# Kernel tuning notes

Measured on AMD Instinct MI355X. Metric: run time of the kernel, lower is better.

Reference implementation:

```python
import jax, jax.numpy as jnp
import numpy as np

B, S, D = 2, 2048, 2048
HQ, HKV = 32, 8
HD = D // HQ            # head_dim = 64
G = HQ // HKV           # groups = 4
KV_DIM = HKV * HD       # 512


def setup_inputs() -> dict:
    key = jax.random.key(0)
    ks = jax.random.split(key, 5)
    x = jax.random.normal(ks[0], (B, S, D), dtype=jnp.float32)
    W_q = jax.random.normal(ks[1], (D, D), dtype=jnp.float32) * (1.0 / np.sqrt(D))
    W_k = jax.random.normal(ks[2], (D, KV_DIM), dtype=jnp.float32) * (1.0 / np.sqrt(D))
    W_v = jax.random.normal(ks[3], (D, KV_DIM), dtype=jnp.float32) * (1.0 / np.sqrt(D))
    W_o = jax.random.normal(ks[4], (D, D), dtype=jnp.float32) * (1.0 / np.sqrt(D))
    # causal mask: 1 where attending allowed, 0 elsewhere (masked_fill(mask==0, -inf))
    mask = jnp.tril(jnp.ones((S, S), dtype=jnp.int32))[None, None, :, :]
    return {"x": x, "W_q": W_q, "W_k": W_k, "W_v": W_v, "W_o": W_o, "mask": mask}


def reference(x, W_q, W_k, W_v, W_o, mask):
    scale = np.sqrt(HD).astype(np.float32)
    # projections
    Q = (x @ W_q).reshape(B, S, HQ, HD).transpose(0, 2, 1, 3)    # (B,Hq,S,hd)
    K = (x @ W_k).reshape(B, S, HKV, HD).transpose(0, 2, 1, 3)   # (B,Hkv,S,hd)
    V = (x @ W_v).reshape(B, S, HKV, HD).transpose(0, 2, 1, 3)   # (B,Hkv,S,hd)
    # group Q heads with their shared KV head instead of repeat_interleave
    Qg = Q.reshape(B, HKV, G, S, HD)                             # (B,Hkv,G,S,hd)
    scores = jnp.einsum('bkgsd,bktd->bkgst', Qg, K) / scale      # (B,Hkv,G,S,T)
    m = mask.reshape(1, 1, 1, S, S)
    scores = jnp.where(m == 0, jnp.float32(-jnp.inf), scores)
    attn = jax.nn.softmax(scores, axis=-1)                       # dropout p=0.0
    out_h = jnp.einsum('bkgst,bktd->bkgsd', attn, V)             # (B,Hkv,G,S,hd)
    out_h = out_h.reshape(B, HQ, S, HD).transpose(0, 2, 1, 3).reshape(B, S, D)
    out = out_h @ W_o
    return out, K, V
```

## Files before the change

kernel.cpp:

```cpp
#include <hip/hip_runtime.h>

typedef unsigned short u16;
typedef unsigned int u32;
typedef __attribute__((ext_vector_type(8))) __bf16 bf16x8;
typedef __attribute__((ext_vector_type(8))) u16 u16x8;
typedef __attribute__((ext_vector_type(2))) u32 u32x2;
typedef __attribute__((ext_vector_type(4))) float f32x4;
typedef __attribute__((ext_vector_type(16))) float f32x16;

#define DEVI static __device__ __forceinline__


DEVI u16 f2bf(float f) {
  unsigned u = __float_as_uint(f);
  u += 0x7fff + ((u >> 16) & 1);
  return (u16)(u >> 16);
}

DEVI u32 cvt_pk_bf16(float lo, float hi) {
  u32 r;
  asm("v_cvt_pk_bf16_f32 %0, %1, %2" : "=v"(r) : "v"(lo), "v"(hi));
  return r;
}

DEVI float bperm_f(int srclane, float v) {
  return __int_as_float(__builtin_amdgcn_ds_bpermute(srclane << 2, __float_as_int(v)));
}

DEVI void gll16(const void* g, void* l) {
  __builtin_amdgcn_global_load_lds((const __attribute__((address_space(1))) void*)g,
                                   (__attribute__((address_space(3))) void*)l, 16, 0, 0);
}

DEVI void stage128x32(const u16* g, int ld, u16* lds) {
  int t = threadIdx.x, w = t >> 6, l = t & 63;
#pragma unroll
  for (int r = 0; r < 2; ++r) {
    int c = (w * 2 + r) * 64 + l;
    int row = c >> 2;
    int p = (c & 3) ^ (row & 3);
    gll16(g + (size_t)row * ld + p * 8, (char*)lds + (w * 2 + r) * 1024);
  }
}

DEVI void stage64x64(const u16* g, int ld, u16* lds) {
  int t = threadIdx.x, w = t >> 6, l = t & 63;
#pragma unroll
  for (int r = 0; r < 2; ++r) {
    int c = (w * 2 + r) * 64 + l;
    int row = c >> 3;
    int p = (c & 7) ^ (row & 7);
    gll16(g + (size_t)row * ld + p * 8, (char*)lds + (w * 2 + r) * 1024);
  }
}

DEVI void gemm_tile(const u16* A, int lda, const u16* Bt, int ldb, int K,
                    int m0, int n0, u16* sA, u16* sB, f32x4 acc[4][4]) {
  const int t = threadIdx.x, w = t >> 6, lane = t & 63;
  const int wr = w >> 1, wc = w & 1, g = lane >> 4, r16 = lane & 15;
  int offa[4], offb[4];
#pragma unroll
  for (int m = 0; m < 4; ++m) {
    int row = wr * 64 + m * 16 + r16;
    offa[m] = row * 32 + ((g ^ (row & 3)) << 3);
  }
#pragma unroll
  for (int n = 0; n < 4; ++n) {
    int row = wc * 64 + n * 16 + r16;
    offb[n] = row * 32 + ((g ^ (row & 3)) << 3);
  }
#pragma unroll
  for (int m = 0; m < 4; ++m)
#pragma unroll
    for (int n = 0; n < 4; ++n) acc[m][n] = f32x4{0.f, 0.f, 0.f, 0.f};

  const u16* At = A + (size_t)m0 * lda;
  const u16* Bb = Bt + (size_t)n0 * ldb;
  stage128x32(At, lda, sA);
  stage128x32(Bb, ldb, sB);
  asm volatile("s_waitcnt vmcnt(0)" ::: "memory");
  __syncthreads();
  const int nk = K >> 5;
  int cur = 0;
  for (int kt = 0; kt < nk; ++kt) {
    if (kt + 1 < nk) {
      stage128x32(At + (kt + 1) * 32, lda, sA + (cur ^ 1) * 4096);
      stage128x32(Bb + (kt + 1) * 32, ldb, sB + (cur ^ 1) * 4096);
    }
    bf16x8 av[4], bv[4];
#pragma unroll
    for (int m = 0; m < 4; ++m) av[m] = *(const bf16x8*)(sA + cur * 4096 + offa[m]);
#pragma unroll
    for (int n = 0; n < 4; ++n) bv[n] = *(const bf16x8*)(sB + cur * 4096 + offb[n]);
#pragma unroll
    for (int m = 0; m < 4; ++m)
#pragma unroll
      for (int n = 0; n < 4; ++n)
        acc[m][n] = __builtin_amdgcn_mfma_f32_16x16x32_bf16(av[m], bv[n], acc[m][n], 0, 0, 0);
    asm volatile("s_waitcnt vmcnt(0)" ::: "memory");
    __syncthreads();
    cur ^= 1;
  }
}

__global__ __launch_bounds__(256) void cvt_kernel(const float* __restrict__ src,
                                                  u16* __restrict__ dst) {
  int i = blockIdx.x * 256 + threadIdx.x;
  float4 a = ((const float4*)src)[2 * i];
  float4 b = ((const float4*)src)[2 * i + 1];
  u16x8 o;
  o[0] = f2bf(a.x); o[1] = f2bf(a.y); o[2] = f2bf(a.z); o[3] = f2bf(a.w);
  o[4] = f2bf(b.x); o[5] = f2bf(b.y); o[6] = f2bf(b.z); o[7] = f2bf(b.w);
  ((u16x8*)dst)[i] = o;
}

__global__ __launch_bounds__(256) void transpose_all(
    const float* __restrict__ wq, const float* __restrict__ wk,
    const float* __restrict__ wv, const float* __restrict__ wo,
    u16* __restrict__ wqT, u16* __restrict__ wkT,
    u16* __restrict__ wvT, u16* __restrict__ woT) {
  __shared__ float tle[32][33];
  int bxr = blockIdx.x;
  const float* src; u16* dst; int C, bxl;
  if (bxr < 64)       { src = wq; dst = wqT; C = 2048; bxl = bxr; }
  else if (bxr < 80)  { src = wk; dst = wkT; C = 512;  bxl = bxr - 64; }
  else if (bxr < 96)  { src = wv; dst = wvT; C = 512;  bxl = bxr - 80; }
  else                { src = wo; dst = woT; C = 2048; bxl = bxr - 96; }
  int bx = bxl * 32, by = blockIdx.y * 32;
  int tx = threadIdx.x, ty = threadIdx.y;
#pragma unroll
  for (int i = 0; i < 32; i += 8) tle[ty + i][tx] = src[(size_t)(by + ty + i) * C + bx + tx];
  __syncthreads();
#pragma unroll
  for (int i = 0; i < 32; i += 8)
    dst[(size_t)(bx + ty + i) * 2048 + by + tx] = f2bf(tle[tx][ty + i]);
}

__global__ __launch_bounds__(256) void proj_kernel(
    const u16* __restrict__ x, const u16* __restrict__ wqT, const u16* __restrict__ wkT,
    const u16* __restrict__ wvT, u16* __restrict__ qout, float* __restrict__ koutf,
    u16* __restrict__ kbf, float* __restrict__ voutf, u16* __restrict__ vtout) {
  __shared__ __align__(16) u16 sA[2 * 4096];
  __shared__ __align__(16) u16 sB[2 * 4096];
  const int bid = blockIdx.x;
  int mode, bm, bn;
  const u16* Bt;
  if (bid < 512) { mode = 0; bm = bid >> 4; bn = bid & 15; Bt = wqT; }
  else if (bid < 640) { mode = 1; int i = bid - 512; bm = i >> 2; bn = i & 3; Bt = wkT; }
  else { mode = 2; int i = bid - 640; bm = i >> 2; bn = i & 3; Bt = wvT; }

  f32x4 acc[4][4];
  gemm_tile(x, 2048, Bt, 2048, 2048, bm * 128, bn * 128, sA, sB, acc);

  const int t = threadIdx.x, w = t >> 6, lane = t & 63;
  const int wr = w >> 1, wc = w & 1, g = lane >> 4, r16 = lane & 15;
  const float QSCALE = 0.125f * 1.44269504088896340736f;
#pragma unroll
  for (int m = 0; m < 4; ++m)
#pragma unroll
    for (int n = 0; n < 4; ++n)
#pragma unroll
      for (int j = 0; j < 4; ++j) {
        int row = bm * 128 + wr * 64 + m * 16 + g * 4 + j;
        int col = bn * 128 + wc * 64 + n * 16 + r16;
        float v = acc[m][n][j];
        if (mode == 0) {
          qout[(size_t)row * 2048 + col] = f2bf(v * QSCALE);
        } else {
          int b = row >> 11, s = row & 2047;
          int h = col >> 6, d = col & 63;
          size_t idx = ((size_t)(b * 8 + h) * 2048 + s) * 64 + d;
          if (mode == 1) {
            koutf[idx] = v;
            kbf[idx] = f2bf(v);
          } else {
            voutf[idx] = v;
            vtout[((size_t)(b * 8 + h) * 64 + d) * 2048 + s] = f2bf(v);
          }
        }
      }
}

DEVI void attn_tile32(const u16* sKc, const u16* sVc, u16* sPw,
                      const bf16x8 (&qf)[4], f32x16 (&accO0)[1], f32x16 (&accO1)[1],
                      float &mi, float &li,
                      int wrow0, int kv0, int lane,
                      const int (&offk)[2][4], const int (&offv)[4][2],
                      const int (&offp)[4]) {
  if (kv0 > wrow0 + 31) return;
  const int l5 = lane >> 5, l31 = lane & 31;
  f32x16 st[2];
#pragma unroll
  for (int i = 0; i < 16; ++i) { st[0][i] = 0.f; st[1][i] = 0.f; }
  __builtin_amdgcn_s_setprio(1);
#pragma unroll
  for (int kd = 0; kd < 4; ++kd)
#pragma unroll
    for (int kb = 0; kb < 2; ++kb) {
      bf16x8 kf = *(const bf16x8*)(sKc + offk[kb][kd]);
      st[kb] = __builtin_amdgcn_mfma_f32_32x32x16_bf16(kf, qf[kd], st[kb], 0, 0, 0);
    }
  __builtin_amdgcn_s_setprio(0);
  if (kv0 + 63 > wrow0) {
    int qg = wrow0 + l31;
#pragma unroll
    for (int kb = 0; kb < 2; ++kb)
#pragma unroll
      for (int r = 0; r < 16; ++r) {
        int kvg = kv0 + kb * 32 + (r & 3) + 8 * (r >> 2) + 4 * l5;
        if (kvg > qg) st[kb][r] = -1e30f;
      }
  }
  float pmax = st[0][0];
#pragma unroll
  for (int r = 1; r < 16; ++r) pmax = fmaxf(pmax, st[0][r]);
#pragma unroll
  for (int r = 0; r < 16; ++r) pmax = fmaxf(pmax, st[1][r]);
  pmax = fmaxf(pmax, __shfl_xor(pmax, 32));
  if (!__all(pmax - mi <= 8.0f)) {
    float mn = fmaxf(mi, pmax);
    float scl = exp2f(mi - mn);
    mi = mn; li *= scl;
#pragma unroll
    for (int r = 0; r < 16; ++r) {
      int qp = (r & 3) + 8 * (r >> 2) + 4 * l5;
      float sj = bperm_f(qp, scl);
      accO0[0][r] *= sj;
      accO1[0][r] *= sj;
    }
  }
  float rs = 0.f;
#pragma unroll
  for (int kb = 0; kb < 2; ++kb)
#pragma unroll
    for (int r = 0; r < 16; ++r) { st[kb][r] = exp2f(st[kb][r] - mi); rs += st[kb][r]; }
  rs += __shfl_xor(rs, 32);
  li += rs;
  {
    u16* base = sPw + l31 * 64;
#pragma unroll
    for (int kb = 0; kb < 2; ++kb)
#pragma unroll
      for (int tt = 0; tt < 4; ++tt) {
        u32 lo = cvt_pk_bf16(st[kb][4 * tt + 0], st[kb][4 * tt + 1]);
        u32 hi = cvt_pk_bf16(st[kb][4 * tt + 2], st[kb][4 * tt + 3]);
        int chunk = kb * 4 + tt;
        u32x2 w2 = {lo, hi};
        *(u32x2*)(base + ((chunk ^ (l31 & 7)) << 3) + l5 * 4) = w2;
      }
  }
  asm volatile("s_waitcnt lgkmcnt(0)" ::: "memory");
  __builtin_amdgcn_s_setprio(1);
#pragma unroll
  for (int ks = 0; ks < 4; ++ks) {
    bf16x8 pa = *(const bf16x8*)(sPw + offp[ks]);
    bf16x8 v0 = *(const bf16x8*)(sVc + offv[ks][0]);
    bf16x8 v1 = *(const bf16x8*)(sVc + offv[ks][1]);
    accO0[0] = __builtin_amdgcn_mfma_f32_32x32x16_bf16(pa, v0, accO0[0], 0, 0, 0);
    accO1[0] = __builtin_amdgcn_mfma_f32_32x32x16_bf16(pa, v1, accO1[0], 0, 0, 0);
  }
  __builtin_amdgcn_s_setprio(0);
}

__global__ __launch_bounds__(256) void attn_kernel(
    const u16* __restrict__ Q, const u16* __restrict__ Kp,
    const u16* __restrict__ Vt, u16* __restrict__ Oh) {
  __shared__ __align__(16) u16 sK[2][4096];
  __shared__ __align__(16) u16 sV[2][4096];
  __shared__ __align__(16) u16 sP[4][2048];
  const int blk = blockIdx.x;
  const int bh = (blk & 7) * 8 + ((blk >> 3) & 7);
  const int bx = blk >> 6;
  const int qbhi = 15 - bx, qblo = bx;
  const int b = bh >> 5, h = bh & 31, hkv = h >> 2;
  const int t = threadIdx.x, w = t >> 6, lane = t & 63;
  const int l5 = lane >> 5, l31 = lane & 31;
  const int wrow_hi = qbhi * 128 + w * 32;
  const int wrow_lo = qblo * 128 + w * 32;

  int offk[2][4], offv[4][2], offp[4];
#pragma unroll
  for (int kb = 0; kb < 2; ++kb) {
    int row = kb * 32 + l31;
#pragma unroll
    for (int kd = 0; kd < 4; ++kd)
      offk[kb][kd] = row * 64 + (((kd * 2 + l5) ^ (row & 7)) << 3);
  }
#pragma unroll
  for (int ks = 0; ks < 4; ++ks) {
    offp[ks] = l31 * 64 + (((ks * 2 + l5) ^ (l31 & 7)) << 3);
#pragma unroll
    for (int nd = 0; nd < 2; ++nd) {
      int rd = nd * 32 + l31;
      offv[ks][nd] = rd * 64 + (((ks * 2 + l5) ^ (rd & 7)) << 3);
    }
  }

  const u16* Qb = Q + (size_t)b * 2048 * 2048 + h * 64 + l5 * 8;
  bf16x8 qfh[4], qfl[4];
#pragma unroll
  for (int kd = 0; kd < 4; ++kd) {
    qfh[kd] = *(const bf16x8*)(Qb + (size_t)(wrow_hi + l31) * 2048 + kd * 16);
    qfl[kd] = *(const bf16x8*)(Qb + (size_t)(wrow_lo + l31) * 2048 + kd * 16);
  }

  const u16* Kh = Kp + (size_t)(b * 8 + hkv) * 2048 * 64;
  const u16* Vh = Vt + (size_t)(b * 8 + hkv) * 64 * 2048;

  f32x16 aoh0[1], aoh1[1], aol0[1], aol1[1];
#pragma unroll
  for (int i = 0; i < 16; ++i) { aoh0[0][i] = 0.f; aoh1[0][i] = 0.f; aol0[0][i] = 0.f; aol1[0][i] = 0.f; }
  float mih = -1e30f, lih = 0.f, mil = -1e30f, lil = 0.f;

  const int nt_hi = 2 * (qbhi + 1), nt_lo = 2 * (qblo + 1);
  int cur = 0;
  stage64x64(Kh, 64, sK[0]);
  stage64x64(Vh, 2048, sV[0]);
  for (int it = 0; it < nt_hi; ++it) {
    asm volatile("s_waitcnt vmcnt(0)" ::: "memory");
    __syncthreads();
    if (it + 1 < nt_hi) {
      stage64x64(Kh + (size_t)(it + 1) * 64 * 64, 64, sK[cur ^ 1]);
      stage64x64(Vh + (it + 1) * 64, 2048, sV[cur ^ 1]);
    }
    const int kv0 = it * 64;
    attn_tile32(sK[cur], sV[cur], sP[w], qfh, aoh0, aoh1, mih, lih, wrow_hi, kv0, lane, offk, offv, offp);
    if (it < nt_lo)
      attn_tile32(sK[cur], sV[cur], sP[w], qfl, aol0, aol1, mil, lil, wrow_lo, kv0, lane, offk, offv, offp);
    cur ^= 1;
  }
  float rlh = 1.0f / lih, rll = 1.0f / lil;
#pragma unroll
  for (int r = 0; r < 16; ++r) {
    int qp = (r & 3) + 8 * (r >> 2) + 4 * l5;
    float fh = bperm_f(qp, rlh);
    float fl = bperm_f(qp, rll);
    size_t rowh = (size_t)b * 2048 + wrow_hi + qp;
    size_t rowl = (size_t)b * 2048 + wrow_lo + qp;
    int col = h * 64 + l31;
    Oh[rowh * 2048 + col]      = f2bf(aoh0[0][r] * fh);
    Oh[rowh * 2048 + col + 32] = f2bf(aoh1[0][r] * fh);
    Oh[rowl * 2048 + col]      = f2bf(aol0[0][r] * fl);
    Oh[rowl * 2048 + col + 32] = f2bf(aol1[0][r] * fl);
  }
}

__global__ __launch_bounds__(256) void outproj_kernel(const u16* __restrict__ A,
                                                      const u16* __restrict__ WoT,
                                                      float* __restrict__ out) {
  __shared__ __align__(16) u16 sA[2 * 4096];
  __shared__ __align__(16) u16 sB[2 * 4096];
  const int bm = blockIdx.x >> 4, bn = blockIdx.x & 15;
  f32x4 acc[4][4];
  gemm_tile(A, 2048, WoT, 2048, 2048, bm * 128, bn * 128, sA, sB, acc);
  const int t = threadIdx.x, w = t >> 6, lane = t & 63;
  const int wr = w >> 1, wc = w & 1, g = lane >> 4, r16 = lane & 15;
#pragma unroll
  for (int m = 0; m < 4; ++m)
#pragma unroll
    for (int n = 0; n < 4; ++n)
#pragma unroll
      for (int j = 0; j < 4; ++j) {
        int row = bm * 128 + wr * 64 + m * 16 + g * 4 + j;
        int col = bn * 128 + wc * 64 + n * 16 + r16;
        out[(size_t)row * 2048 + col] = acc[m][n][j];
      }
}

extern "C" void kernel_launch(void* const* d_in, const int* in_sizes, int n_in,
                              void* d_out, int out_size, void* d_ws, size_t ws_size,
                              hipStream_t stream) {
  const float* x  = (const float*)d_in[0];
  const float* wq = (const float*)d_in[1];
  const float* wk = (const float*)d_in[2];
  const float* wv = (const float*)d_in[3];
  const float* wo = (const float*)d_in[4];

  const size_t NEED_BYTES = 2ull * (8388608 + 4194304 + 1048576 + 1048576 + 4194304);
  if (ws_size < NEED_BYTES) return;

  float* outf  = (float*)d_out;
  float* koutf = outf + (size_t)8388608;
  float* voutf = koutf + (size_t)2097152;

  u16* Qs  = (u16*)d_out;
  u16* Vt  = Qs + (size_t)8388608;
  u16* Kbf = Vt + (size_t)2097152;

  u16* ws   = (u16*)d_ws;
  u16* xbf  = ws;
  u16* Oh   = ws;
  u16* wqT  = ws  + (size_t)8388608;
  u16* wkT  = wqT + (size_t)4194304;
  u16* wvT  = wkT + (size_t)1048576;
  u16* woT  = wvT + (size_t)1048576;

  cvt_kernel<<<4096, 256, 0, stream>>>(x, xbf);
  transpose_all<<<dim3(160, 64), dim3(32, 8), 0, stream>>>(wq, wk, wv, wo, wqT, wkT, wvT, woT);

  proj_kernel<<<768, 256, 0, stream>>>(xbf, wqT, wkT, wvT, Qs, koutf, Kbf, voutf, Vt);
  attn_kernel<<<512, 256, 0, stream>>>(Qs, Kbf, Vt, Oh);
  outproj_kernel<<<512, 256, 0, stream>>>(Oh, woT, outf);
}
```

Measured before the change: 282.4 us.

## Split paired causal q-blocks into separate workgroups with XCD-aware head mapping

Each attention workgroup previously handled two q-blocks (one high, one low) so that causal work was balanced per block. Now each workgroup handles a single q-block, which doubles the grid to 1024. Blocks are ordered longest-first, and the four query heads sharing a KV head are placed on the same XCD so they can reuse K/V in L2. This trades the built-in load balancing and the shared K/V staging of the old pairing for more parallelism and lower register pressure per workgroup. Balance now depends on the hardware scheduler handling the longest-first ordering well.

```diff
diff --git a/kernel.cpp b/kernel.cpp
--- a/kernel.cpp
+++ b/kernel.cpp
@@ -268,15 +268,16 @@
   __shared__ __align__(16) u16 sK[2][4096];
   __shared__ __align__(16) u16 sV[2][4096];
   __shared__ __align__(16) u16 sP[4][2048];
-  const int blk = blockIdx.x;
-  const int bh = (blk & 7) * 8 + ((blk >> 3) & 7);
-  const int bx = blk >> 6;
-  const int qbhi = 15 - bx, qblo = bx;
-  const int b = bh >> 5, h = bh & 31, hkv = h >> 2;
+  const int bid = blockIdx.x;
+  const int xcd = bid & 7, rank = bid >> 3;
+  const int qb = 15 - (rank >> 3);
+  const int sub = rank & 7;
+  const int bhkv = xcd * 2 + (sub >> 2);
+  const int b = bhkv >> 3, hkv = bhkv & 7;
+  const int h = hkv * 4 + (sub & 3);
   const int t = threadIdx.x, w = t >> 6, lane = t & 63;
   const int l5 = lane >> 5, l31 = lane & 31;
-  const int wrow_hi = qbhi * 128 + w * 32;
-  const int wrow_lo = qblo * 128 + w * 32;
+  const int wrow0 = qb * 128 + w * 32;
 
   int offk[2][4], offv[4][2], offp[4];
 #pragma unroll
@@ -297,51 +298,43 @@
   }
 
   const u16* Qb = Q + (size_t)b * 2048 * 2048 + h * 64 + l5 * 8;
-  bf16x8 qfh[4], qfl[4];
-#pragma unroll
-  for (int kd = 0; kd < 4; ++kd) {
-    qfh[kd] = *(const bf16x8*)(Qb + (size_t)(wrow_hi + l31) * 2048 + kd * 16);
-    qfl[kd] = *(const bf16x8*)(Qb + (size_t)(wrow_lo + l31) * 2048 + kd * 16);
-  }
+  bf16x8 qf[4];
+#pragma unroll
+  for (int kd = 0; kd < 4; ++kd)
+    qf[kd] = *(const bf16x8*)(Qb + (size_t)(wrow0 + l31) * 2048 + kd * 16);
 
   const u16* Kh = Kp + (size_t)(b * 8 + hkv) * 2048 * 64;
   const u16* Vh = Vt + (size_t)(b * 8 + hkv) * 64 * 2048;
 
-  f32x16 aoh0[1], aoh1[1], aol0[1], aol1[1];
-#pragma unroll
-  for (int i = 0; i < 16; ++i) { aoh0[0][i] = 0.f; aoh1[0][i] = 0.f; aol0[0][i] = 0.f; aol1[0][i] = 0.f; }
-  float mih = -1e30f, lih = 0.f, mil = -1e30f, lil = 0.f;
-
-  const int nt_hi = 2 * (qbhi + 1), nt_lo = 2 * (qblo + 1);
+  f32x16 ao0[1], ao1[1];
+#pragma unroll
+  for (int i = 0; i < 16; ++i) { ao0[0][i] = 0.f; ao1[0][i] = 0.f; }
+  float mi = -1e30f, li = 0.f;
+
+  const int nt = 2 * (qb + 1);
   int cur = 0;
   stage64x64(Kh, 64, sK[0]);
   stage64x64(Vh, 2048, sV[0]);
-  for (int it = 0; it < nt_hi; ++it) {
+  for (int it = 0; it < nt; ++it) {
     asm volatile("s_waitcnt vmcnt(0)" ::: "memory");
     __syncthreads();
-    if (it + 1 < nt_hi) {
+    if (it + 1 < nt) {
       stage64x64(Kh + (size_t)(it + 1) * 64 * 64, 64, sK[cur ^ 1]);
       stage64x64(Vh + (it + 1) * 64, 2048, sV[cur ^ 1]);
     }
     const int kv0 = it * 64;
-    attn_tile32(sK[cur], sV[cur], sP[w], qfh, aoh0, aoh1, mih, lih, wrow_hi, kv0, lane, offk, offv, offp);
-    if (it < nt_lo)
-      attn_tile32(sK[cur], sV[cur], sP[w], qfl, aol0, aol1, mil, lil, wrow_lo, kv0, lane, offk, offv, offp);
+    attn_tile32(sK[cur], sV[cur], sP[w], qf, ao0, ao1, mi, li, wrow0, kv0, lane, offk, offv, offp);
     cur ^= 1;
   }
-  float rlh = 1.0f / lih, rll = 1.0f / lil;
+  float rl = 1.0f / li;
 #pragma unroll
   for (int r = 0; r < 16; ++r) {
     int qp = (r & 3) + 8 * (r >> 2) + 4 * l5;
-    float fh = bperm_f(qp, rlh);
-    float fl = bperm_f(qp, rll);
-    size_t rowh = (size_t)b * 2048 + wrow_hi + qp;
-    size_t rowl = (size_t)b * 2048 + wrow_lo + qp;
+    float f = bperm_f(qp, rl);
+    size_t row = (size_t)b * 2048 + wrow0 + qp;
     int col = h * 64 + l31;
-    Oh[rowh * 2048 + col]      = f2bf(aoh0[0][r] * fh);
-    Oh[rowh * 2048 + col + 32] = f2bf(aoh1[0][r] * fh);
-    Oh[rowl * 2048 + col]      = f2bf(aol0[0][r] * fl);
-    Oh[rowl * 2048 + col + 32] = f2bf(aol1[0][r] * fl);
+    Oh[row * 2048 + col]      = f2bf(ao0[0][r] * f);
+    Oh[row * 2048 + col + 32] = f2bf(ao1[0][r] * f);
   }
 }
 
@@ -399,6 +392,6 @@
   transpose_all<<<dim3(160, 64), dim3(32, 8), 0, stream>>>(wq, wk, wv, wo, wqT, wkT, wvT, woT);
 
   proj_kernel<<<768, 256, 0, stream>>>(xbf, wqT, wkT, wvT, Qs, koutf, Kbf, voutf, Vt);
-  attn_kernel<<<512, 256, 0, stream>>>(Qs, Kbf, Vt, Oh);
+  attn_kernel<<<1024, 256, 0, stream>>>(Qs, Kbf, Vt, Oh);
   outproj_kernel<<<512, 256, 0, stream>>>(Oh, woT, outf);
 }
```

After: 233.8 us. 1.21x faster.
